# Kernel optimization log

Measured on AMD Instinct MI355X. Metric: run time of the kernel, lower is better.

The kernel has to match this reference:

```python
import jax, jax.numpy as jnp
import numpy as np

ALPHA = 1.5        # router_alpha
TEMP = 1.0         # router_temperature
N_ITER = 25        # bisection iterations (entmax_bisect default in module)
THRESH = 1e-9      # activation_threshold


def entmax_bisect(X, alpha=ALPHA, n_iter=N_ITER):
    """alpha-entmax over last axis via bisection (matches entmax.entmax_bisect)."""
    d = X.shape[-1]
    inv_am1 = 1.0 / (alpha - 1.0)
    Xs = X * (alpha - 1.0)
    max_val = jnp.max(Xs, axis=-1, keepdims=True)
    tau_lo = max_val - 1.0                                   # gp_inv(1) = 1
    tau_hi = max_val - (1.0 / d) ** (alpha - 1.0)            # gp_inv(1/d)
    f_lo = jnp.sum(jnp.maximum(Xs - tau_lo, 0.0) ** inv_am1, axis=-1, keepdims=True) - 1.0

    def body(i, carry):
        tau_lo, dm, _ = carry
        dm = dm * 0.5
        tau_m = tau_lo + dm
        f_m = jnp.sum(jnp.maximum(Xs - tau_m, 0.0) ** inv_am1, axis=-1, keepdims=True) - 1.0
        tau_lo = jnp.where(f_m * f_lo >= 0.0, tau_m, tau_lo)
        return (tau_lo, dm, tau_m)

    dm0 = tau_hi - tau_lo
    _, _, tau_m = jax.lax.fori_loop(0, n_iter, body, (tau_lo, dm0, tau_lo))
    p = jnp.maximum(Xs - tau_m, 0.0) ** inv_am1
    return p / jnp.sum(p, axis=-1, keepdims=True)


def setup_inputs() -> dict:
    key = jax.random.key(0)
    ks = jax.random.split(key, 8)
    B, S, D, E = 2, 1024, 1024, 8
    F = 4 * D
    return {
        "x":  jax.random.normal(ks[0], (B, S, D), jnp.float32),
        "Wr": jax.random.normal(ks[1], (D, E), jnp.float32) * 0.02,
        "br": jnp.zeros((E,), jnp.float32),
        "W1": jax.random.normal(ks[2], (E, D, F), jnp.float32) * 0.02,
        "b1": jnp.zeros((E, F), jnp.float32),
        "W2": jax.random.normal(ks[3], (E, F, D), jnp.float32) * 0.02,
        "b2": jnp.zeros((E, D), jnp.float32),
    }


def reference(x, Wr, br, W1, b1, W2, b2):
    B, S, D = x.shape
    xt = x.reshape(B * S, D)                       # [T, D]
    logits = (xt @ Wr + br) / TEMP                 # [T, E]
    gates = entmax_bisect(logits)                  # sparse alpha-entmax gates
    # tokens with gate <= threshold are skipped in the torch loop -> zero contribution
    gates = jnp.where(gates > THRESH, gates, 0.0)
    # dense-equivalent of per-expert gather -> FFN -> weighted scatter-add
    h = jax.nn.relu(jnp.einsum('td,edf->etf', xt, W1) + b1[:, None, :])   # [E, T, 4D]
    y = jnp.einsum('etf,efd->etd', h, W2) + b2[:, None, :]                # [E, T, D]
    out = jnp.einsum('etd,te->td', y, gates)       # gate-weighted combine
    return out.reshape(B, S, D)
```

## Files before the change

### kernel.cpp

```cpp
#include <hip/hip_runtime.h>
#include <hip/hip_bf16.h>
#include <stdint.h>

#define DDIM 1024
#define EXP 8
#define FDIM 4096
#define BK 32
#define LDT 40

typedef __attribute__((ext_vector_type(8))) short bf16x8;
typedef __attribute__((ext_vector_type(8))) short short8v;
typedef __attribute__((ext_vector_type(4))) short short4v;
typedef __attribute__((ext_vector_type(4))) float f32x4;

__device__ __forceinline__ unsigned short f2bf(float f) {
    unsigned u = __float_as_uint(f);
    u += 0x7FFFu + ((u >> 16) & 1u);
    return (unsigned short)(u >> 16);
}
__device__ __forceinline__ float bf2f(unsigned short h) {
    return __uint_as_float(((unsigned)h) << 16);
}

__global__ __launch_bounds__(256) void splitx_kernel(
    const float* __restrict__ x, unsigned short* __restrict__ Xh,
    unsigned short* __restrict__ Xl, int total4)
{
    int i = blockIdx.x * 256 + threadIdx.x;
    if (i >= total4) return;
    float4 v = ((const float4*)x)[i];
    float f[4] = {v.x, v.y, v.z, v.w};
    short4v h4, l4;
#pragma unroll
    for (int j = 0; j < 4; ++j) {
        unsigned short hh = f2bf(f[j]);
        h4[j] = (short)hh;
        l4[j] = (short)f2bf(f[j] - bf2f(hh));
    }
    ((short4v*)Xh)[i] = h4;
    ((short4v*)Xl)[i] = l4;
}

__global__ __launch_bounds__(256) void router_kernel(
    const float* __restrict__ x, const float* __restrict__ Wr,
    const float* __restrict__ br, const float* __restrict__ b2,
    float* __restrict__ gates, float* __restrict__ Gb2)
{
    const int t = blockIdx.x;
    const int tid = threadIdx.x;
    const float* xr = x + (size_t)t * DDIM;

    float acc[EXP];
#pragma unroll
    for (int e = 0; e < EXP; ++e) acc[e] = 0.f;
    for (int d = tid; d < DDIM; d += 256) {
        float xv = xr[d];
        const float* wr = Wr + (size_t)d * EXP;
#pragma unroll
        for (int e = 0; e < EXP; ++e) acc[e] += xv * wr[e];
    }
#pragma unroll
    for (int e = 0; e < EXP; ++e) {
        float v = acc[e];
#pragma unroll
        for (int off = 32; off > 0; off >>= 1) v += __shfl_down(v, off);
        acc[e] = v;
    }
    __shared__ float part[4][EXP];
    __shared__ float gsh[EXP];
    const int wave = tid >> 6, lane = tid & 63;
    if (lane == 0) {
#pragma unroll
        for (int e = 0; e < EXP; ++e) part[wave][e] = acc[e];
    }
    __syncthreads();

    if (tid == 0) {
        float Xs[EXP];
        float mx = -1e30f;
#pragma unroll
        for (int e = 0; e < EXP; ++e) {
            float lg = part[0][e] + part[1][e] + part[2][e] + part[3][e] + br[e];
            Xs[e] = 0.5f * lg;
            mx = fmaxf(mx, Xs[e]);
        }
        float tau_lo = mx - 1.0f;
        const float tau_hi = mx - 0.35355339059327373f;
        float f_lo = -1.0f;
#pragma unroll
        for (int e = 0; e < EXP; ++e) {
            float u = fmaxf(Xs[e] - tau_lo, 0.f);
            f_lo += u * u;
        }
        float dm = tau_hi - tau_lo;
        float tau_m = tau_lo;
        for (int it = 0; it < 25; ++it) {
            dm *= 0.5f;
            tau_m = tau_lo + dm;
            float f_m = -1.0f;
#pragma unroll
            for (int e = 0; e < EXP; ++e) {
                float u = fmaxf(Xs[e] - tau_m, 0.f);
                f_m += u * u;
            }
            if (f_m * f_lo >= 0.f) tau_lo = tau_m;
        }
        float p[EXP], s = 0.f;
#pragma unroll
        for (int e = 0; e < EXP; ++e) {
            float u = fmaxf(Xs[e] - tau_m, 0.f);
            p[e] = u * u;
            s += p[e];
        }
        float inv = 1.f / s;
#pragma unroll
        for (int e = 0; e < EXP; ++e) {
            float g = p[e] * inv;
            g = (g > 1e-9f) ? g : 0.f;
            gates[(size_t)t * EXP + e] = g;
            gsh[e] = g;
        }
    }
    __syncthreads();

    const int d = tid * 4;
    float4 s4 = {0.f, 0.f, 0.f, 0.f};
#pragma unroll
    for (int e = 0; e < EXP; ++e) {
        float g = gsh[e];
        float4 bb = *(const float4*)(b2 + (size_t)e * DDIM + d);
        s4.x += g * bb.x; s4.y += g * bb.y; s4.z += g * bb.z; s4.w += g * bb.w;
    }
    *(float4*)(Gb2 + (size_t)t * DDIM + d) = s4;
}

template<int EPI>
__global__ __launch_bounds__(256) void gemm_kernel(
    const unsigned short* __restrict__ Ah, const unsigned short* __restrict__ Al,
    int lda, const float* __restrict__ W, int K, int N,
    const float* __restrict__ bias, const float* __restrict__ gates,
    unsigned short* __restrict__ Oh, unsigned short* __restrict__ Ol,
    float* __restrict__ P, int CT, int t0)
{
    const int e  = blockIdx.z;
    const int m0 = blockIdx.x * 128;
    const int n0 = blockIdx.y * 128;
    const int tid = threadIdx.x;
    const int lane = tid & 63;
    const int wid = tid >> 6;
    const int wr = wid >> 1, wc = wid & 1;

    __shared__ unsigned short sAh[128 * LDT], sAl[128 * LDT];
    __shared__ unsigned short sBh[128 * LDT], sBl[128 * LDT];

    const float* Wg = W + (size_t)e * K * N;
    const long abase = (EPI == 1) ? (long)t0 : (long)e * CT;

    const int am = tid >> 1;
    const int ak = (tid & 1) * 16;
    const unsigned short* Agh = Ah + (size_t)(abase + m0 + am) * lda + ak;
    const unsigned short* Agl = Al + (size_t)(abase + m0 + am) * lda + ak;

    const int bk = (tid & 7) * 4;
    const int bn = ((tid >> 3) & 31) * 4;
    const float* Bg = Wg + (size_t)bk * N + n0 + bn;

    f32x4 acc[4][4];
#pragma unroll
    for (int mi = 0; mi < 4; ++mi)
#pragma unroll
        for (int ni = 0; ni < 4; ++ni) acc[mi][ni] = (f32x4){0.f, 0.f, 0.f, 0.f};

    const int lr = lane & 15, lg = lane >> 4;

    for (int kt = 0; kt < K; kt += BK) {
        short8v a_h0 = *(const short8v*)(Agh + kt);
        short8v a_h1 = *(const short8v*)(Agh + kt + 8);
        short8v a_l0 = *(const short8v*)(Agl + kt);
        short8v a_l1 = *(const short8v*)(Agl + kt + 8);
        float4 bv[4];
#pragma unroll
        for (int i = 0; i < 4; ++i)
            bv[i] = *(const float4*)(Bg + (size_t)(kt + i) * N);

        __syncthreads();

        *(short8v*)&sAh[am * LDT + ak]     = a_h0;
        *(short8v*)&sAh[am * LDT + ak + 8] = a_h1;
        *(short8v*)&sAl[am * LDT + ak]     = a_l0;
        *(short8v*)&sAl[am * LDT + ak + 8] = a_l1;

#pragma unroll
        for (int j = 0; j < 4; ++j) {
            short4v h4, l4;
#pragma unroll
            for (int i = 0; i < 4; ++i) {
                float f = ((const float*)&bv[i])[j];
                unsigned short hh = f2bf(f);
                h4[i] = (short)hh;
                l4[i] = (short)f2bf(f - bf2f(hh));
            }
            *(short4v*)&sBh[(bn + j) * LDT + bk] = h4;
            *(short4v*)&sBl[(bn + j) * LDT + bk] = l4;
        }
        __syncthreads();

        bf16x8 afh[4], afl[4];
#pragma unroll
        for (int mi = 0; mi < 4; ++mi) {
            int row = wr * 64 + mi * 16 + lr;
            afh[mi] = *(const bf16x8*)&sAh[row * LDT + lg * 8];
            afl[mi] = *(const bf16x8*)&sAl[row * LDT + lg * 8];
        }
#pragma unroll
        for (int ni = 0; ni < 4; ++ni) {
            int col = wc * 64 + ni * 16 + lr;
            bf16x8 bfh = *(const bf16x8*)&sBh[col * LDT + lg * 8];
            bf16x8 bfl = *(const bf16x8*)&sBl[col * LDT + lg * 8];
#pragma unroll
            for (int mi = 0; mi < 4; ++mi) {
                acc[mi][ni] = __builtin_amdgcn_mfma_f32_16x16x32_bf16(afh[mi], bfh, acc[mi][ni], 0, 0, 0);
                acc[mi][ni] = __builtin_amdgcn_mfma_f32_16x16x32_bf16(afh[mi], bfl, acc[mi][ni], 0, 0, 0);
                acc[mi][ni] = __builtin_amdgcn_mfma_f32_16x16x32_bf16(afl[mi], bfh, acc[mi][ni], 0, 0, 0);
            }
        }
    }

#pragma unroll
    for (int mi = 0; mi < 4; ++mi) {
#pragma unroll
        for (int ni = 0; ni < 4; ++ni) {
            const int col = n0 + wc * 64 + ni * 16 + lr;
#pragma unroll
            for (int r = 0; r < 4; ++r) {
                const int mrow = m0 + wr * 64 + mi * 16 + lg * 4 + r;
                float v = acc[mi][ni][r];
                if (EPI == 1) {
                    float g = gates[(size_t)(t0 + mrow) * EXP + e];
                    v = fmaxf(v + bias[(size_t)e * FDIM + col], 0.f) * g;
                    unsigned short hh = f2bf(v);
                    size_t idx = ((size_t)e * CT + mrow) * FDIM + col;
                    Oh[idx] = hh;
                    Ol[idx] = f2bf(v - bf2f(hh));
                } else {
                    P[((size_t)e * CT + mrow) * DDIM + col] = v;
                }
            }
        }
    }
}

__global__ __launch_bounds__(256) void reduce_kernel(
    const float* __restrict__ P, const float* __restrict__ Gb2,
    float* __restrict__ out, int t0, int CT)
{
    int i = blockIdx.x * 256 + threadIdx.x;
    int total4 = CT * DDIM / 4;
    if (i >= total4) return;
    size_t goff = (size_t)t0 * DDIM / 4 + i;
    float4 s = ((const float4*)Gb2)[goff];
#pragma unroll
    for (int e = 0; e < EXP; ++e) {
        float4 p = ((const float4*)P)[(size_t)e * CT * DDIM / 4 + i];
        s.x += p.x; s.y += p.y; s.z += p.z; s.w += p.w;
    }
    ((float4*)out)[goff] = s;
}

extern "C" void kernel_launch(void* const* d_in, const int* in_sizes, int n_in,
                              void* d_out, int out_size, void* d_ws, size_t ws_size,
                              hipStream_t stream)
{
    const float* x  = (const float*)d_in[0];
    const float* Wr = (const float*)d_in[1];
    const float* br = (const float*)d_in[2];
    const float* W1 = (const float*)d_in[3];
    const float* b1 = (const float*)d_in[4];
    const float* W2 = (const float*)d_in[5];
    const float* b2 = (const float*)d_in[6];
    float* out = (float*)d_out;

    const int T = in_sizes[0] / DDIM;

    char* p = (char*)d_ws;
    size_t used = 0;
    auto carve = [&](size_t bytes) {
        char* r = p + used;
        used += (bytes + 255) & ~(size_t)255;
        return r;
    };
    float* gates = (float*)carve((size_t)T * EXP * 4);
    float* Gb2   = (float*)carve((size_t)T * DDIM * 4);
    unsigned short* Xh = (unsigned short*)carve((size_t)T * DDIM * 2);
    unsigned short* Xl = (unsigned short*)carve((size_t)T * DDIM * 2);

    const size_t per_tok = (size_t)EXP * FDIM * 4 + (size_t)EXP * DDIM * 4;
    size_t avail = (ws_size > used) ? (ws_size - used) : 0;
    int CT = 128;
    for (int c = 2048; c >= 128; c >>= 1) {
        if ((size_t)c * per_tok + 1024 <= avail) { CT = c; break; }
    }
    if (CT > T) CT = T;
    unsigned short* Hh = (unsigned short*)carve((size_t)EXP * CT * FDIM * 2);
    unsigned short* Hl = (unsigned short*)carve((size_t)EXP * CT * FDIM * 2);
    float*          Pp = (float*)carve((size_t)EXP * CT * DDIM * 4);

    const int total4x = T * DDIM / 4;
    splitx_kernel<<<dim3((total4x + 255) / 256), dim3(256), 0, stream>>>(x, Xh, Xl, total4x);
    router_kernel<<<dim3(T), dim3(256), 0, stream>>>(x, Wr, br, b2, gates, Gb2);

    for (int t0 = 0; t0 < T; t0 += CT) {
        dim3 g1(CT / 128, FDIM / 128, EXP);
        gemm_kernel<1><<<g1, dim3(256), 0, stream>>>(
            Xh, Xl, DDIM, W1, DDIM, FDIM, b1, gates, Hh, Hl, (float*)nullptr, CT, t0);
        dim3 g2(CT / 128, DDIM / 128, EXP);
        gemm_kernel<2><<<g2, dim3(256), 0, stream>>>(
            Hh, Hl, FDIM, W2, FDIM, DDIM, (const float*)nullptr, (const float*)nullptr,
            (unsigned short*)nullptr, (unsigned short*)nullptr, Pp, CT, t0);
        reduce_kernel<<<dim3((CT * DDIM / 4 + 255) / 256), dim3(256), 0, stream>>>(
            Pp, Gb2, out, t0, CT);
    }
}
```

Before: 1.348 ms.

## Pre-pack operands into swizzled bf16 hi/lo tiles and stream them directly into LDS

Adds pack kernels that split x, W1 and W2 into bf16 hi/lo pairs once per call. They are stored in tile-contiguous, XOR-swizzled 16KB blocks, so the GEMM no longer converts fp32 weights inside its K loop. The GEMM now loads tiles with global_load_lds, uses a 1D grid remapped across XCDs, and writes its first-layer output straight into the same packed layout. The b2 gate-weighted bias is folded into the reduce kernel. In exchange it adds full-weight repacking passes every call and needs much more workspace, which could shrink the token chunk size.

```diff
diff --git a/kernel.cpp b/kernel.cpp
--- a/kernel.cpp
+++ b/kernel.cpp
@@ -5,12 +5,9 @@
 #define DDIM 1024
 #define EXP 8
 #define FDIM 4096
-#define BK 32
-#define LDT 40
-
+
+typedef __attribute__((ext_vector_type(8))) short short8v;
 typedef __attribute__((ext_vector_type(8))) short bf16x8;
-typedef __attribute__((ext_vector_type(8))) short short8v;
-typedef __attribute__((ext_vector_type(4))) short short4v;
 typedef __attribute__((ext_vector_type(4))) float f32x4;
 
 __device__ __forceinline__ unsigned short f2bf(float f) {
@@ -22,29 +19,73 @@
     return __uint_as_float(((unsigned)h) << 16);
 }
 
-__global__ __launch_bounds__(256) void splitx_kernel(
-    const float* __restrict__ x, unsigned short* __restrict__ Xh,
-    unsigned short* __restrict__ Xl, int total4)
-{
-    int i = blockIdx.x * 256 + threadIdx.x;
-    if (i >= total4) return;
-    float4 v = ((const float4*)x)[i];
-    float f[4] = {v.x, v.y, v.z, v.w};
-    short4v h4, l4;
+
+__global__ __launch_bounds__(256) void packx_kernel(
+    const float* __restrict__ x, char* __restrict__ Xp, int T)
+{
+    int idx = blockIdx.x * 256 + threadIdx.x;
+    int r = idx >> 7;
+    int k8 = idx & 127;
+    if (r >= T) return;
+    const float* src = x + (size_t)r * DDIM + k8 * 8;
+    float4 v0 = *(const float4*)(src);
+    float4 v1 = *(const float4*)(src + 4);
+    float f[8] = {v0.x, v0.y, v0.z, v0.w, v1.x, v1.y, v1.z, v1.w};
+    short8v h8, l8;
+#pragma unroll
+    for (int i = 0; i < 8; ++i) {
+        unsigned short hh = f2bf(f[i]);
+        h8[i] = (short)hh;
+        l8[i] = (short)f2bf(f[i] - bf2f(hh));
+    }
+    int kb = k8 >> 2, k8l = k8 & 3, rl = r & 127, rb = r >> 7;
+    size_t tb = ((size_t)(rb * (DDIM >> 5) + kb)) << 14;
+    char* dst = Xp + tb + (rl << 7);
+    int sh = (k8l ^ (rl & 7)) << 4;
+    *(short8v*)(dst + sh) = h8;
+    *(short8v*)(dst + (sh ^ 64)) = l8;
+}
+
+__global__ __launch_bounds__(256) void packw_kernel(
+    const float* __restrict__ W, char* __restrict__ Wp, int K, int N)
+{
+    int kb = blockIdx.x, nb = blockIdx.y, e = blockIdx.z;
+    int t = threadIdx.x;
+    int Ktiles = K >> 5;
+    __shared__ float lds[32][132];
+    const float* src = W + (size_t)e * K * N + (size_t)(kb * 32) * N + nb * 128;
 #pragma unroll
     for (int j = 0; j < 4; ++j) {
-        unsigned short hh = f2bf(f[j]);
-        h4[j] = (short)hh;
-        l4[j] = (short)f2bf(f[j] - bf2f(hh));
-    }
-    ((short4v*)Xh)[i] = h4;
-    ((short4v*)Xl)[i] = l4;
+        int idx = t + j * 256;
+        int kk = idx >> 5, c4 = idx & 31;
+        float4 v = *(const float4*)(src + (size_t)kk * N + c4 * 4);
+        *(float4*)&lds[kk][c4 * 4] = v;
+    }
+    __syncthreads();
+    int n = t >> 1, pair = t & 1;
+    char* dstrow = Wp + (size_t)e * ((size_t)N * K * 4)
+                 + (((size_t)(nb * Ktiles + kb)) << 14) + (n << 7);
+    int nx = n & 7;
+#pragma unroll
+    for (int q = 0; q < 2; ++q) {
+        int k8 = pair * 2 + q;
+        short8v h8, l8;
+#pragma unroll
+        for (int i = 0; i < 8; ++i) {
+            float f = lds[k8 * 8 + i][n];
+            unsigned short hh = f2bf(f);
+            h8[i] = (short)hh;
+            l8[i] = (short)f2bf(f - bf2f(hh));
+        }
+        int sh = (k8 ^ nx) << 4;
+        *(short8v*)(dstrow + sh) = h8;
+        *(short8v*)(dstrow + (sh ^ 64)) = l8;
+    }
 }
 
 __global__ __launch_bounds__(256) void router_kernel(
     const float* __restrict__ x, const float* __restrict__ Wr,
-    const float* __restrict__ br, const float* __restrict__ b2,
-    float* __restrict__ gates, float* __restrict__ Gb2)
+    const float* __restrict__ br, float* __restrict__ gates)
 {
     const int t = blockIdx.x;
     const int tid = threadIdx.x;
@@ -67,7 +108,6 @@
         acc[e] = v;
     }
     __shared__ float part[4][EXP];
-    __shared__ float gsh[EXP];
     const int wave = tid >> 6, lane = tid & 63;
     if (lane == 0) {
 #pragma unroll
@@ -116,54 +156,42 @@
 #pragma unroll
         for (int e = 0; e < EXP; ++e) {
             float g = p[e] * inv;
-            g = (g > 1e-9f) ? g : 0.f;
-            gates[(size_t)t * EXP + e] = g;
-            gsh[e] = g;
-        }
-    }
-    __syncthreads();
-
-    const int d = tid * 4;
-    float4 s4 = {0.f, 0.f, 0.f, 0.f};
-#pragma unroll
-    for (int e = 0; e < EXP; ++e) {
-        float g = gsh[e];
-        float4 bb = *(const float4*)(b2 + (size_t)e * DDIM + d);
-        s4.x += g * bb.x; s4.y += g * bb.y; s4.z += g * bb.z; s4.w += g * bb.w;
-    }
-    *(float4*)(Gb2 + (size_t)t * DDIM + d) = s4;
+            gates[(size_t)t * EXP + e] = (g > 1e-9f) ? g : 0.f;
+        }
+    }
 }
 
 template<int EPI>
-__global__ __launch_bounds__(256) void gemm_kernel(
-    const unsigned short* __restrict__ Ah, const unsigned short* __restrict__ Al,
-    int lda, const float* __restrict__ W, int K, int N,
+__global__ __launch_bounds__(256) void gemm_pk(
+    const char* __restrict__ Ap, size_t a_es, int arb0,
+    const char* __restrict__ Bp, size_t b_es,
+    int Ktiles, int Mb, int Nb,
     const float* __restrict__ bias, const float* __restrict__ gates,
-    unsigned short* __restrict__ Oh, unsigned short* __restrict__ Ol,
-    float* __restrict__ P, int CT, int t0)
-{
-    const int e  = blockIdx.z;
-    const int m0 = blockIdx.x * 128;
-    const int n0 = blockIdx.y * 128;
+    char* __restrict__ Hout, float* __restrict__ Pout,
+    int CT, int t0)
+{
+    __shared__ char sA[16384];
+    __shared__ char sB[16384];
+
     const int tid = threadIdx.x;
     const int lane = tid & 63;
     const int wid = tid >> 6;
     const int wr = wid >> 1, wc = wid & 1;
-
-    __shared__ unsigned short sAh[128 * LDT], sAl[128 * LDT];
-    __shared__ unsigned short sBh[128 * LDT], sBl[128 * LDT];
-
-    const float* Wg = W + (size_t)e * K * N;
-    const long abase = (EPI == 1) ? (long)t0 : (long)e * CT;
-
-    const int am = tid >> 1;
-    const int ak = (tid & 1) * 16;
-    const unsigned short* Agh = Ah + (size_t)(abase + m0 + am) * lda + ak;
-    const unsigned short* Agl = Al + (size_t)(abase + m0 + am) * lda + ak;
-
-    const int bk = (tid & 7) * 4;
-    const int bn = ((tid >> 3) & 31) * 4;
-    const float* Bg = Wg + (size_t)bk * N + n0 + bn;
+    const int lr = lane & 15, lg = lane >> 4;
+    const int rx = lr & 7;
+
+    int bI = blockIdx.x;
+    int nwg = Mb * Nb * EXP;
+    int cpx = nwg >> 3;
+    int w = (bI & 7) * cpx + (bI >> 3);
+    int e = w / (Mb * Nb);
+    int rem = w - e * (Mb * Nb);
+    int mb, nb;
+    if (EPI == 1) { nb = rem / Mb; mb = rem - nb * Mb; }
+    else          { mb = rem / Nb; nb = rem - mb * Nb; }
+
+    const char* Abase = Ap + (size_t)e * a_es + (((size_t)(arb0 + mb) * Ktiles) << 14);
+    const char* Bbase = Bp + (size_t)e * b_es + (((size_t)nb * Ktiles) << 14);
 
     f32x4 acc[4][4];
 #pragma unroll
@@ -171,100 +199,120 @@
 #pragma unroll
         for (int ni = 0; ni < 4; ++ni) acc[mi][ni] = (f32x4){0.f, 0.f, 0.f, 0.f};
 
-    const int lr = lane & 15, lg = lane >> 4;
-
-    for (int kt = 0; kt < K; kt += BK) {
-        short8v a_h0 = *(const short8v*)(Agh + kt);
-        short8v a_h1 = *(const short8v*)(Agh + kt + 8);
-        short8v a_l0 = *(const short8v*)(Agl + kt);
-        short8v a_l1 = *(const short8v*)(Agl + kt + 8);
-        float4 bv[4];
-#pragma unroll
-        for (int i = 0; i < 4; ++i)
-            bv[i] = *(const float4*)(Bg + (size_t)(kt + i) * N);
-
+    int aoff[4], boff[4];
+#pragma unroll
+    for (int mi = 0; mi < 4; ++mi)
+        aoff[mi] = (wr * 64 + mi * 16 + lr) * 128 + ((lg ^ rx) << 4);
+#pragma unroll
+    for (int ni = 0; ni < 4; ++ni)
+        boff[ni] = (wc * 64 + ni * 16 + lr) * 128 + ((lg ^ rx) << 4);
+
+    const int stg = (wid << 12) + (lane << 4);
+    const int ldst = wid << 12;
+
+    for (int kb = 0; kb < Ktiles; ++kb) {
+        const char* at = Abase + ((size_t)kb << 14) + stg;
+        const char* bt = Bbase + ((size_t)kb << 14) + stg;
         __syncthreads();
-
-        *(short8v*)&sAh[am * LDT + ak]     = a_h0;
-        *(short8v*)&sAh[am * LDT + ak + 8] = a_h1;
-        *(short8v*)&sAl[am * LDT + ak]     = a_l0;
-        *(short8v*)&sAl[am * LDT + ak + 8] = a_l1;
-
 #pragma unroll
         for (int j = 0; j < 4; ++j) {
-            short4v h4, l4;
-#pragma unroll
-            for (int i = 0; i < 4; ++i) {
-                float f = ((const float*)&bv[i])[j];
-                unsigned short hh = f2bf(f);
-                h4[i] = (short)hh;
-                l4[i] = (short)f2bf(f - bf2f(hh));
+            __builtin_amdgcn_global_load_lds(
+                (const __attribute__((address_space(1))) void*)(at + j * 1024),
+                (__attribute__((address_space(3))) void*)(sA + ldst + j * 1024),
+                16, 0, 0);
+            __builtin_amdgcn_global_load_lds(
+                (const __attribute__((address_space(1))) void*)(bt + j * 1024),
+                (__attribute__((address_space(3))) void*)(sB + ldst + j * 1024),
+                16, 0, 0);
+        }
+        __syncthreads();
+
+        bf16x8 ah[4], al[4];
+#pragma unroll
+        for (int mi = 0; mi < 4; ++mi) {
+            ah[mi] = *(const bf16x8*)(sA + aoff[mi]);
+            al[mi] = *(const bf16x8*)(sA + (aoff[mi] ^ 64));
+        }
+#pragma unroll
+        for (int ni = 0; ni < 4; ++ni) {
+            bf16x8 bh = *(const bf16x8*)(sB + boff[ni]);
+            bf16x8 bl = *(const bf16x8*)(sB + (boff[ni] ^ 64));
+#pragma unroll
+            for (int mi = 0; mi < 4; ++mi) {
+                acc[mi][ni] = __builtin_amdgcn_mfma_f32_16x16x32_bf16(ah[mi], bh, acc[mi][ni], 0, 0, 0);
+                acc[mi][ni] = __builtin_amdgcn_mfma_f32_16x16x32_bf16(ah[mi], bl, acc[mi][ni], 0, 0, 0);
+                acc[mi][ni] = __builtin_amdgcn_mfma_f32_16x16x32_bf16(al[mi], bh, acc[mi][ni], 0, 0, 0);
             }
-            *(short4v*)&sBh[(bn + j) * LDT + bk] = h4;
-            *(short4v*)&sBl[(bn + j) * LDT + bk] = l4;
-        }
-        __syncthreads();
-
-        bf16x8 afh[4], afl[4];
-#pragma unroll
-        for (int mi = 0; mi < 4; ++mi) {
-            int row = wr * 64 + mi * 16 + lr;
-            afh[mi] = *(const bf16x8*)&sAh[row * LDT + lg * 8];
-            afl[mi] = *(const bf16x8*)&sAl[row * LDT + lg * 8];
-        }
+        }
+    }
+
+    const int m0 = mb * 128, n0 = nb * 128;
+    if (EPI == 1) {
+        char* He = Hout + (size_t)e * ((size_t)CT * FDIM * 4);
+        float garr[4][4];
+#pragma unroll
+        for (int mi = 0; mi < 4; ++mi)
+#pragma unroll
+            for (int r = 0; r < 4; ++r)
+                garr[mi][r] = gates[(size_t)(t0 + m0 + wr * 64 + mi * 16 + lg * 4 + r) * EXP + e];
 #pragma unroll
         for (int ni = 0; ni < 4; ++ni) {
-            int col = wc * 64 + ni * 16 + lr;
-            bf16x8 bfh = *(const bf16x8*)&sBh[col * LDT + lg * 8];
-            bf16x8 bfl = *(const bf16x8*)&sBl[col * LDT + lg * 8];
+            const int f = n0 + wc * 64 + ni * 16 + lr;
+            const float bv = bias[e * FDIM + f];
+            const int fb = f >> 5, kl = f & 31;
 #pragma unroll
             for (int mi = 0; mi < 4; ++mi) {
-                acc[mi][ni] = __builtin_amdgcn_mfma_f32_16x16x32_bf16(afh[mi], bfh, acc[mi][ni], 0, 0, 0);
-                acc[mi][ni] = __builtin_amdgcn_mfma_f32_16x16x32_bf16(afh[mi], bfl, acc[mi][ni], 0, 0, 0);
-                acc[mi][ni] = __builtin_amdgcn_mfma_f32_16x16x32_bf16(afl[mi], bfh, acc[mi][ni], 0, 0, 0);
-            }
-        }
-    }
-
-#pragma unroll
-    for (int mi = 0; mi < 4; ++mi) {
-#pragma unroll
-        for (int ni = 0; ni < 4; ++ni) {
-            const int col = n0 + wc * 64 + ni * 16 + lr;
-#pragma unroll
-            for (int r = 0; r < 4; ++r) {
-                const int mrow = m0 + wr * 64 + mi * 16 + lg * 4 + r;
-                float v = acc[mi][ni][r];
-                if (EPI == 1) {
-                    float g = gates[(size_t)(t0 + mrow) * EXP + e];
-                    v = fmaxf(v + bias[(size_t)e * FDIM + col], 0.f) * g;
+#pragma unroll
+                for (int r = 0; r < 4; ++r) {
+                    int mrow = m0 + wr * 64 + mi * 16 + lg * 4 + r;
+                    float v = fmaxf(acc[mi][ni][r] + bv, 0.f) * garr[mi][r];
                     unsigned short hh = f2bf(v);
-                    size_t idx = ((size_t)e * CT + mrow) * FDIM + col;
-                    Oh[idx] = hh;
-                    Ol[idx] = f2bf(v - bf2f(hh));
-                } else {
-                    P[((size_t)e * CT + mrow) * DDIM + col] = v;
+                    unsigned short ll = f2bf(v - bf2f(hh));
+                    int rl = mrow & 127;
+                    size_t tb = ((size_t)((mrow >> 7) * (FDIM >> 5) + fb)) << 14;
+                    char* pa = He + tb + (rl << 7) + ((kl & 7) << 1);
+                    int sh = (((kl >> 3) ^ (rl & 7)) << 4);
+                    *(unsigned short*)(pa + sh) = hh;
+                    *(unsigned short*)(pa + (sh ^ 64)) = ll;
                 }
             }
         }
+    } else {
+#pragma unroll
+        for (int mi = 0; mi < 4; ++mi) {
+#pragma unroll
+            for (int ni = 0; ni < 4; ++ni) {
+                const int col = n0 + wc * 64 + ni * 16 + lr;
+#pragma unroll
+                for (int r = 0; r < 4; ++r) {
+                    int mrow = m0 + wr * 64 + mi * 16 + lg * 4 + r;
+                    Pout[((size_t)e * CT + mrow) * DDIM + col] = acc[mi][ni][r];
+                }
+            }
+        }
     }
 }
 
 __global__ __launch_bounds__(256) void reduce_kernel(
-    const float* __restrict__ P, const float* __restrict__ Gb2,
-    float* __restrict__ out, int t0, int CT)
+    const float* __restrict__ P, const float* __restrict__ gates,
+    const float* __restrict__ b2, float* __restrict__ out, int t0, int CT)
 {
     int i = blockIdx.x * 256 + threadIdx.x;
-    int total4 = CT * DDIM / 4;
-    if (i >= total4) return;
-    size_t goff = (size_t)t0 * DDIM / 4 + i;
-    float4 s = ((const float4*)Gb2)[goff];
+    int m = i >> 8, d4 = i & 255;
+    if (m >= CT) return;
+    int t = t0 + m;
+    float4 s = {0.f, 0.f, 0.f, 0.f};
 #pragma unroll
     for (int e = 0; e < EXP; ++e) {
-        float4 p = ((const float4*)P)[(size_t)e * CT * DDIM / 4 + i];
-        s.x += p.x; s.y += p.y; s.z += p.z; s.w += p.w;
-    }
-    ((float4*)out)[goff] = s;
+        float g = gates[(size_t)t * EXP + e];
+        float4 p = ((const float4*)P)[((size_t)e * CT + m) * 256 + d4];
+        float4 bb = ((const float4*)b2)[e * 256 + d4];
+        s.x += p.x + g * bb.x;
+        s.y += p.y + g * bb.y;
+        s.z += p.z + g * bb.z;
+        s.w += p.w + g * bb.w;
+    }
+    ((float4*)out)[(size_t)t * 256 + d4] = s;
 }
 
 extern "C" void kernel_launch(void* const* d_in, const int* in_sizes, int n_in,
@@ -290,34 +338,32 @@
         return r;
     };
     float* gates = (float*)carve((size_t)T * EXP * 4);
-    float* Gb2   = (float*)carve((size_t)T * DDIM * 4);
-    unsigned short* Xh = (unsigned short*)carve((size_t)T * DDIM * 2);
-    unsigned short* Xl = (unsigned short*)carve((size_t)T * DDIM * 2);
+    char*  Xp    = carve((size_t)T * DDIM * 4);
+    char*  W1p   = carve((size_t)EXP * DDIM * FDIM * 4);
+    char*  W2p   = carve((size_t)EXP * FDIM * DDIM * 4);
 
     const size_t per_tok = (size_t)EXP * FDIM * 4 + (size_t)EXP * DDIM * 4;
-    size_t avail = (ws_size > used) ? (ws_size - used) : 0;
     int CT = 128;
-    for (int c = 2048; c >= 128; c >>= 1) {
-        if ((size_t)c * per_tok + 1024 <= avail) { CT = c; break; }
-    }
+    for (int c = 2048; c >= 128; c >>= 1)
+        if (used + (size_t)c * per_tok + 1024 <= ws_size) { CT = c; break; }
     if (CT > T) CT = T;
-    unsigned short* Hh = (unsigned short*)carve((size_t)EXP * CT * FDIM * 2);
-    unsigned short* Hl = (unsigned short*)carve((size_t)EXP * CT * FDIM * 2);
-    float*          Pp = (float*)carve((size_t)EXP * CT * DDIM * 4);
-
-    const int total4x = T * DDIM / 4;
-    splitx_kernel<<<dim3((total4x + 255) / 256), dim3(256), 0, stream>>>(x, Xh, Xl, total4x);
-    router_kernel<<<dim3(T), dim3(256), 0, stream>>>(x, Wr, br, b2, gates, Gb2);
-
+    char*  Hp = carve((size_t)EXP * CT * FDIM * 4);
+    float* Pp = (float*)carve((size_t)EXP * CT * DDIM * 4);
+
+    packx_kernel<<<dim3((T * (DDIM / 8) + 255) / 256), dim3(256), 0, stream>>>(x, Xp, T);
+    packw_kernel<<<dim3(DDIM / 32, FDIM / 128, EXP), dim3(256), 0, stream>>>(W1, W1p, DDIM, FDIM);
+    packw_kernel<<<dim3(FDIM / 32, DDIM / 128, EXP), dim3(256), 0, stream>>>(W2, W2p, FDIM, DDIM);
+    router_kernel<<<dim3(T), dim3(256), 0, stream>>>(x, Wr, br, gates);
+
+    const size_t w_es = (size_t)DDIM * FDIM * 4;
     for (int t0 = 0; t0 < T; t0 += CT) {
-        dim3 g1(CT / 128, FDIM / 128, EXP);
-        gemm_kernel<1><<<g1, dim3(256), 0, stream>>>(
-            Xh, Xl, DDIM, W1, DDIM, FDIM, b1, gates, Hh, Hl, (float*)nullptr, CT, t0);
-        dim3 g2(CT / 128, DDIM / 128, EXP);
-        gemm_kernel<2><<<g2, dim3(256), 0, stream>>>(
-            Hh, Hl, FDIM, W2, FDIM, DDIM, (const float*)nullptr, (const float*)nullptr,
-            (unsigned short*)nullptr, (unsigned short*)nullptr, Pp, CT, t0);
-        reduce_kernel<<<dim3((CT * DDIM / 4 + 255) / 256), dim3(256), 0, stream>>>(
-            Pp, Gb2, out, t0, CT);
-    }
-}
+        int Mb = CT / 128;
+        gemm_pk<1><<<dim3(Mb * (FDIM / 128) * EXP), dim3(256), 0, stream>>>(
+            Xp, (size_t)0, t0 >> 7, W1p, w_es, DDIM / 32, Mb, FDIM / 128,
+            b1, gates, Hp, (float*)nullptr, CT, t0);
+        gemm_pk<2><<<dim3(Mb * (DDIM / 128) * EXP), dim3(256), 0, stream>>>(
+            Hp, (size_t)CT * FDIM * 4, 0, W2p, w_es, FDIM / 32, Mb, DDIM / 128,
+            (const float*)nullptr, gates, (char*)nullptr, Pp, CT, t0);
+        reduce_kernel<<<dim3(CT), dim3(256), 0, stream>>>(Pp, gates, b2, out, t0, CT);
+    }
+}
```

Result: slower. 1.470 ms (+9.0%).
